# Performance work log

Measured on AMD Instinct MI355X. Metric: run time of the kernel, lower is better.

Reference implementation:

```python
import jax, jax.numpy as jnp
import numpy as np

B, T, S_ENC, D, H, E, K = 4, 1024, 64, 1024, 16, 8, 2
DK = D // H
HID = 4 * D
NEG = -65504.0
EPS = 1e-5


def rmsnorm(x, w):
    return w * (x * jax.lax.rsqrt(jnp.mean(x * x, axis=-1, keepdims=True) + EPS))


def mha(xq, xk, xv, mask, wq, wk, wv, wo):
    # linear (no bias): y = x @ W.T
    q = jnp.einsum('bsd,ed->bse', xq, wq).reshape(xq.shape[0], -1, H, DK).transpose(0, 2, 1, 3)
    k = jnp.einsum('bsd,ed->bse', xk, wk).reshape(xk.shape[0], -1, H, DK).transpose(0, 2, 1, 3)
    v = jnp.einsum('bsd,ed->bse', xv, wv).reshape(xv.shape[0], -1, H, DK).transpose(0, 2, 1, 3)
    scores = jnp.einsum('bhqd,bhkd->bhqk', q, k) / jnp.sqrt(jnp.float32(DK))
    scores = jnp.where(mask[:, None, :, :] == 0, NEG, scores)
    attn = jax.nn.softmax(scores, axis=-1)
    out = jnp.einsum('bhqk,bhkd->bhqd', attn, v)
    out = out.transpose(0, 2, 1, 3).reshape(xq.shape[0], -1, D)
    return jnp.einsum('bsd,ed->bse', out, wo)


def moe_ffn(x, gate_w, exp_w1, exp_w2, sh_w1, sh_w2):
    b, s, d = x.shape
    xf = x.reshape(-1, d)                                     # [N, D]
    # shared expert
    sh = jnp.einsum('nd,hd->nh', xf, sh_w1)
    sh = jax.nn.silu(sh)
    sh = jnp.einsum('nh,dh->nd', sh, sh_w2)
    # gating
    logits = jnp.einsum('nd,ed->ne', xf, gate_w)              # [N, E]
    topk_vals, topk_idx = jax.lax.top_k(logits, K)
    topk_gates = jax.nn.softmax(topk_vals, axis=-1)
    n = xf.shape[0]
    gates = jnp.zeros((n, E), dtype=xf.dtype).at[jnp.arange(n)[:, None], topk_idx].set(topk_gates)
    # all experts computed densely (as in the torch code), then gated
    h = jnp.einsum('nd,ehd->neh', xf, exp_w1)                 # [N, E, 4D]
    h = jax.nn.silu(h)
    eo = jnp.einsum('neh,edh->ned', h, exp_w2)                # [N, E, D]
    sel = jnp.einsum('ned,ne->nd', eo, gates)
    return (sh + sel).reshape(b, s, d)


def setup_inputs() -> dict:
    key = jax.random.key(0)
    ks = jax.random.split(key, 16)
    sd = 1.0 / np.sqrt(D)
    inp = {
        'x': jax.random.normal(ks[0], (B, T, D), jnp.float32),
        'encoder_output': jax.random.normal(ks[1], (B, S_ENC, D), jnp.float32),
        'tgt_mask': jnp.tril(jnp.ones((T, T), jnp.int32))[None].repeat(B, 0),
        'src_mask': jnp.ones((B, T, S_ENC), jnp.int32),
        'norm1_w': jnp.ones((D,), jnp.float32),
        'norm2_w': jnp.ones((D,), jnp.float32),
        'norm3_w': jnp.ones((D,), jnp.float32),
        'sa_wq': jax.random.normal(ks[2], (D, D), jnp.float32) * sd,
        'sa_wk': jax.random.normal(ks[3], (D, D), jnp.float32) * sd,
        'sa_wv': jax.random.normal(ks[4], (D, D), jnp.float32) * sd,
        'sa_wo': jax.random.normal(ks[5], (D, D), jnp.float32) * sd,
        'ca_wq': jax.random.normal(ks[6], (D, D), jnp.float32) * sd,
        'ca_wk': jax.random.normal(ks[7], (D, D), jnp.float32) * sd,
        'ca_wv': jax.random.normal(ks[8], (D, D), jnp.float32) * sd,
        'ca_wo': jax.random.normal(ks[9], (D, D), jnp.float32) * sd,
        'gate_w': jax.random.normal(ks[10], (E, D), jnp.float32) * 0.02,
        'exp_w1': jax.random.normal(ks[11], (E, HID, D), jnp.float32) * sd,
        'exp_w2': jax.random.normal(ks[12], (E, D, HID), jnp.float32) / np.sqrt(HID),
        'sh_w1': jax.random.normal(ks[13], (HID, D), jnp.float32) * sd,
        'sh_w2': jax.random.normal(ks[14], (D, HID), jnp.float32) / np.sqrt(HID),
    }
    return inp


def reference(x, encoder_output, tgt_mask, src_mask, norm1_w, norm2_w, norm3_w,
              sa_wq, sa_wk, sa_wv, sa_wo, ca_wq, ca_wk, ca_wv, ca_wo,
              gate_w, exp_w1, exp_w2, sh_w1, sh_w2):
    xn = rmsnorm(x, norm1_w)
    h = x + mha(xn, xn, xn, tgt_mask, sa_wq, sa_wk, sa_wv, sa_wo)
    hn = rmsnorm(h, norm2_w)
    h = h + mha(hn, encoder_output, encoder_output, src_mask, ca_wq, ca_wk, ca_wv, ca_wo)
    hn = rmsnorm(h, norm3_w)
    return h + moe_ffn(hn, gate_w, exp_w1, exp_w2, sh_w1, sh_w2)
```

## Files before the change

### kernel.cpp

```cpp
#include <hip/hip_runtime.h>
#include <hip/hip_bf16.h>
#include <cstdint>
#include <cstddef>
#include <math.h>

typedef __attribute__((ext_vector_type(8))) short bf16x8;
typedef __attribute__((ext_vector_type(4))) float f32x4;
typedef __attribute__((ext_vector_type(4))) short s16x4;

static __device__ __forceinline__ short f2bf(float f) {
  union { __hip_bfloat16 b; short s; } u;
  u.b = __float2bfloat16(f);
  return u.s;
}

static __device__ __forceinline__ float bf2f(short s) {
  union { unsigned u; float f; } v;
  v.u = ((unsigned)(unsigned short)s) << 16;
  return v.f;
}

static __device__ __forceinline__ void gload_lds16(const short* g, short* l) {
  __builtin_amdgcn_global_load_lds((const __attribute__((address_space(1))) void*)g,
                                   (__attribute__((address_space(3))) void*)l,
                                   16, 0, 0);
}

__global__ __launch_bounds__(256) void cvt_k(const float* __restrict__ src,
                                             short* __restrict__ dst, long n4) {
  long i = (long)blockIdx.x * blockDim.x + threadIdx.x;
  long stride = (long)gridDim.x * blockDim.x;
  for (; i < n4; i += stride) {
    float4 v = ((const float4*)src)[i];
    s16x4 o;
    o.x = f2bf(v.x); o.y = f2bf(v.y); o.z = f2bf(v.z); o.w = f2bf(v.w);
    ((s16x4*)dst)[i] = o;
  }
}

__global__ __launch_bounds__(256) void cvt2_k(const float* __restrict__ src,
                                              short* __restrict__ hi,
                                              short* __restrict__ lo, long n4) {
  long i = (long)blockIdx.x * blockDim.x + threadIdx.x;
  long stride = (long)gridDim.x * blockDim.x;
  for (; i < n4; i += stride) {
    float4 v = ((const float4*)src)[i];
    s16x4 h, l;
    h.x = f2bf(v.x); l.x = f2bf(v.x - bf2f(h.x));
    h.y = f2bf(v.y); l.y = f2bf(v.y - bf2f(h.y));
    h.z = f2bf(v.z); l.z = f2bf(v.z - bf2f(h.z));
    h.w = f2bf(v.w); l.w = f2bf(v.w - bf2f(h.w));
    ((s16x4*)hi)[i] = h;
    ((s16x4*)lo)[i] = l;
  }
}

__global__ __launch_bounds__(256) void rms2_k(const float* __restrict__ x,
                                              const float* __restrict__ w,
                                              short* __restrict__ hi,
                                              short* __restrict__ lo) {
  const int row = blockIdx.x, tid = threadIdx.x;
  const float* xr = x + (size_t)row * 1024;
  float4 v = *(const float4*)&xr[tid * 4];
  float ss = v.x * v.x + v.y * v.y + v.z * v.z + v.w * v.w;
#pragma unroll
  for (int off = 32; off; off >>= 1) ss += __shfl_down(ss, off);
  __shared__ float red[4];
  if ((tid & 63) == 0) red[tid >> 6] = ss;
  __syncthreads();
  float rs = rsqrtf((red[0] + red[1] + red[2] + red[3]) * (1.f / 1024.f) + 1e-5f);
  float4 wv = *(const float4*)&w[tid * 4];
  float o0 = v.x * rs * wv.x, o1 = v.y * rs * wv.y;
  float o2 = v.z * rs * wv.z, o3 = v.w * rs * wv.w;
  s16x4 h, l;
  h.x = f2bf(o0); l.x = f2bf(o0 - bf2f(h.x));
  h.y = f2bf(o1); l.y = f2bf(o1 - bf2f(h.y));
  h.z = f2bf(o2); l.z = f2bf(o2 - bf2f(h.z));
  h.w = f2bf(o3); l.w = f2bf(o3 - bf2f(h.w));
  const size_t ib = (size_t)row * 1024 + tid * 4;
  *(s16x4*)&hi[ib] = h;
  *(s16x4*)&lo[ib] = l;
}

__global__ __launch_bounds__(256) void rms_k(const float* __restrict__ x,
                                             const float* __restrict__ w,
                                             short* __restrict__ obf) {
  const int row = blockIdx.x, tid = threadIdx.x;
  const float* xr = x + (size_t)row * 1024;
  float4 v = *(const float4*)&xr[tid * 4];
  float ss = v.x * v.x + v.y * v.y + v.z * v.z + v.w * v.w;
#pragma unroll
  for (int off = 32; off; off >>= 1) ss += __shfl_down(ss, off);
  __shared__ float red[4];
  if ((tid & 63) == 0) red[tid >> 6] = ss;
  __syncthreads();
  float rs = rsqrtf((red[0] + red[1] + red[2] + red[3]) * (1.f / 1024.f) + 1e-5f);
  float4 wv = *(const float4*)&w[tid * 4];
  s16x4 ob;
  ob.x = f2bf(v.x * rs * wv.x); ob.y = f2bf(v.y * rs * wv.y);
  ob.z = f2bf(v.z * rs * wv.z); ob.w = f2bf(v.w * rs * wv.w);
  *(s16x4*)&obf[(size_t)row * 1024 + tid * 4] = ob;
}

template <int EPI>
__global__ __launch_bounds__(256)
void gemm3_k(const short* __restrict__ Ah, const short* __restrict__ Al,
             const short* __restrict__ Bh, const short* __restrict__ Bl,
             float* __restrict__ C, const float* __restrict__ resid,
             short* __restrict__ Ch, short* __restrict__ Cl,
             int M, int N, int K) {
  __shared__ short sAh[128 * 32];
  __shared__ short sAl[128 * 32];
  __shared__ short sBh[128 * 32];
  __shared__ short sBl[128 * 32];

  const int bn = blockIdx.x, bm = blockIdx.y;
  const int tid = threadIdx.x;
  const int lane = tid & 63, wv = tid >> 6;
  const int rch = lane >> 2;
  const int cch = (((lane & 3) ^ (rch & 3)) << 3);
  const int wr = wv >> 1, wc = wv & 1;
  const int lr = lane & 15, lg = lane >> 4;
  const int c0 = wv * 2, c1 = wv * 2 + 1;
  const int sw = ((lg ^ (lr & 3)) << 3);

  const int ra0 = bm * 128 + c0 * 16 + rch;
  const int ra1 = bm * 128 + c1 * 16 + rch;
  const int rb0 = bn * 128 + c0 * 16 + rch, rb1 = bn * 128 + c1 * 16 + rch;

  f32x4 acc[4][4];
#pragma unroll
  for (int m = 0; m < 4; m++)
#pragma unroll
    for (int n = 0; n < 4; n++) acc[m][n] = (f32x4){0.f, 0.f, 0.f, 0.f};

  const int nk = K >> 5;
  for (int kt = 0; kt < nk; ++kt) {
    __syncthreads();
    const int colk = (kt << 5) + cch;
    gload_lds16(Ah + (size_t)ra0 * K + colk, &sAh[c0 * 512]);
    gload_lds16(Ah + (size_t)ra1 * K + colk, &sAh[c1 * 512]);
    gload_lds16(Al + (size_t)ra0 * K + colk, &sAl[c0 * 512]);
    gload_lds16(Al + (size_t)ra1 * K + colk, &sAl[c1 * 512]);
    gload_lds16(Bh + (size_t)rb0 * K + colk, &sBh[c0 * 512]);
    gload_lds16(Bh + (size_t)rb1 * K + colk, &sBh[c1 * 512]);
    gload_lds16(Bl + (size_t)rb0 * K + colk, &sBl[c0 * 512]);
    gload_lds16(Bl + (size_t)rb1 * K + colk, &sBl[c1 * 512]);
    __syncthreads();
    bf16x8 ah[4], al[4], bh[4], bl[4];
#pragma unroll
    for (int m = 0; m < 4; m++) {
      const int o = (wr * 64 + m * 16 + lr) * 32 + sw;
      ah[m] = *(const bf16x8*)&sAh[o];
      al[m] = *(const bf16x8*)&sAl[o];
    }
#pragma unroll
    for (int n = 0; n < 4; n++) {
      const int o = (wc * 64 + n * 16 + lr) * 32 + sw;
      bh[n] = *(const bf16x8*)&sBh[o];
      bl[n] = *(const bf16x8*)&sBl[o];
    }
#pragma unroll
    for (int m = 0; m < 4; m++)
#pragma unroll
      for (int n = 0; n < 4; n++) {
        acc[m][n] = __builtin_amdgcn_mfma_f32_16x16x32_bf16(ah[m], bh[n], acc[m][n], 0, 0, 0);
        acc[m][n] = __builtin_amdgcn_mfma_f32_16x16x32_bf16(al[m], bh[n], acc[m][n], 0, 0, 0);
        acc[m][n] = __builtin_amdgcn_mfma_f32_16x16x32_bf16(ah[m], bl[n], acc[m][n], 0, 0, 0);
      }
  }

  const int cbase = bn * 128 + wc * 64;
#pragma unroll
  for (int m = 0; m < 4; m++) {
    const int rl = bm * 128 + wr * 64 + m * 16 + lg * 4;
#pragma unroll
    for (int n = 0; n < 4; n++) {
      f32x4 v = acc[m][n];
      const int col = cbase + n * 16 + lr;
#pragma unroll
      for (int j = 0; j < 4; j++) {
        const size_t idx = (size_t)(rl + j) * N + col;
        if (EPI == 0) {
          C[idx] = v[j];
        } else if (EPI == 2) {
          C[idx] = v[j] + resid[idx];
        } else {
          short hh = f2bf(v[j]);
          Ch[idx] = hh;
          Cl[idx] = f2bf(v[j] - bf2f(hh));
        }
      }
    }
  }
}

template <bool CAUSAL>
__global__ __launch_bounds__(256)
void attn3_k(const short* __restrict__ Qh, const short* __restrict__ Ql, int ldq,
             const short* __restrict__ Kh, const short* __restrict__ Kl, int ldk,
             const short* __restrict__ Vh, const short* __restrict__ Vl, int ldv,
             short* __restrict__ Oh, short* __restrict__ Ol, int ldo,
             int Tq, int Tkv, float scale) {
  __shared__ short sQh[64 * 72], sQl[64 * 72];
  __shared__ short sKh[64 * 72], sKl[64 * 72];
  __shared__ short sVh[64 * 72], sVl[64 * 72];
  __shared__ short sPh[4][16 * 72], sPl[4][16 * 72];

  const int idx = blockIdx.x;
  const int qb = 15 - (idx >> 6);
  const int h = (idx >> 2) & 15;
  const int b = idx & 3;
  const int tid = threadIdx.x, lane = tid & 63, wv = tid >> 6;
  const int hoff = h * 64;
  const int lr = lane & 15, lg = lane >> 4;
  const int qlo = wv * 16;

#pragma unroll
  for (int j = 0; j < 2; j++) {
    int c = j * 256 + tid;
    int row = c >> 3, col = (c & 7) << 3;
    size_t g = (size_t)(b * Tq + qb * 64 + row) * ldq + hoff + col;
    *(bf16x8*)&sQh[row * 72 + col] = *(const bf16x8*)&Qh[g];
    *(bf16x8*)&sQl[row * 72 + col] = *(const bf16x8*)&Ql[g];
  }

  float m_run = -1e30f, l_run = 0.f;
  f32x4 o[4];
#pragma unroll
  for (int n = 0; n < 4; n++) o[n] = (f32x4){0.f, 0.f, 0.f, 0.f};

  const int ntiles = CAUSAL ? (qb + 1) : (Tkv >> 6);
  for (int kt = 0; kt < ntiles; ++kt) {
    __syncthreads();
#pragma unroll
    for (int j = 0; j < 2; j++) {
      int c = j * 256 + tid;
      int row = c >> 3, col = (c & 7) << 3;
      size_t gk = (size_t)(b * Tkv + kt * 64 + row) * ldk + hoff + col;
      *(bf16x8*)&sKh[row * 72 + col] = *(const bf16x8*)&Kh[gk];
      *(bf16x8*)&sKl[row * 72 + col] = *(const bf16x8*)&Kl[gk];
      size_t gv = (size_t)(b * Tkv + kt * 64 + row) * ldv + hoff + col;
      bf16x8 vh = *(const bf16x8*)&Vh[gv];
      bf16x8 vl = *(const bf16x8*)&Vl[gv];
#pragma unroll
      for (int i = 0; i < 8; i++) {
        sVh[(col + i) * 72 + row] = vh[i];
        sVl[(col + i) * 72 + row] = vl[i];
      }
    }
    __syncthreads();

    f32x4 st[4];
#pragma unroll
    for (int jk = 0; jk < 4; jk++) st[jk] = (f32x4){0.f, 0.f, 0.f, 0.f};
#pragma unroll
    for (int ks = 0; ks < 2; ks++) {
      bf16x8 qh = *(const bf16x8*)&sQh[(qlo + lr) * 72 + ks * 32 + lg * 8];
      bf16x8 ql = *(const bf16x8*)&sQl[(qlo + lr) * 72 + ks * 32 + lg * 8];
#pragma unroll
      for (int jk = 0; jk < 4; jk++) {
        const int o2 = (jk * 16 + lr) * 72 + ks * 32 + lg * 8;
        bf16x8 kh = *(const bf16x8*)&sKh[o2];
        bf16x8 kl = *(const bf16x8*)&sKl[o2];
        st[jk] = __builtin_amdgcn_mfma_f32_16x16x32_bf16(kh, qh, st[jk], 0, 0, 0);
        st[jk] = __builtin_amdgcn_mfma_f32_16x16x32_bf16(kl, qh, st[jk], 0, 0, 0);
        st[jk] = __builtin_amdgcn_mfma_f32_16x16x32_bf16(kh, ql, st[jk], 0, 0, 0);
      }
    }

    const int qg = qb * 64 + qlo + lr;
    float s[16];
    float tmax = -1e30f;
#pragma unroll
    for (int jk = 0; jk < 4; jk++)
#pragma unroll
      for (int r2 = 0; r2 < 4; r2++) {
        float xv = st[jk][r2] * scale;
        if (CAUSAL && kt == qb) {
          int kvidx = kt * 64 + jk * 16 + lg * 4 + r2;
          if (kvidx > qg) xv = -1e30f;
        }
        s[jk * 4 + r2] = xv;
        tmax = fmaxf(tmax, xv);
      }
    tmax = fmaxf(tmax, __shfl_xor(tmax, 16));
    tmax = fmaxf(tmax, __shfl_xor(tmax, 32));
    float m_new = fmaxf(m_run, tmax);
    float alpha = __expf(m_run - m_new);
    float tsum = 0.f;
#pragma unroll
    for (int i = 0; i < 16; i++) {
      float ev = (s[i] <= -1e29f) ? 0.f : __expf(s[i] - m_new);
      s[i] = ev;
      tsum += ev;
    }
    tsum += __shfl_xor(tsum, 16);
    tsum += __shfl_xor(tsum, 32);
    l_run = l_run * alpha + tsum;
    m_run = m_new;

    short* pwh = &sPh[wv][0];
    short* pwl = &sPl[wv][0];
#pragma unroll
    for (int jk = 0; jk < 4; jk++) {
      s16x4 ph, pl;
      float e0 = s[jk * 4 + 0], e1 = s[jk * 4 + 1], e2 = s[jk * 4 + 2], e3 = s[jk * 4 + 3];
      ph.x = f2bf(e0); pl.x = f2bf(e0 - bf2f(ph.x));
      ph.y = f2bf(e1); pl.y = f2bf(e1 - bf2f(ph.y));
      ph.z = f2bf(e2); pl.z = f2bf(e2 - bf2f(ph.z));
      ph.w = f2bf(e3); pl.w = f2bf(e3 - bf2f(ph.w));
      *(s16x4*)&pwh[lr * 72 + jk * 16 + lg * 4] = ph;
      *(s16x4*)&pwl[lr * 72 + jk * 16 + lg * 4] = pl;
    }
#pragma unroll
    for (int r2 = 0; r2 < 4; r2++) {
      float al = __shfl(alpha, lg * 4 + r2);
#pragma unroll
      for (int db = 0; db < 4; db++) o[db][r2] *= al;
    }
    __syncthreads();

#pragma unroll
    for (int ks = 0; ks < 2; ks++) {
      bf16x8 pah = *(const bf16x8*)&pwh[lr * 72 + ks * 32 + lg * 8];
      bf16x8 pal = *(const bf16x8*)&pwl[lr * 72 + ks * 32 + lg * 8];
#pragma unroll
      for (int db = 0; db < 4; db++) {
        const int o2 = (db * 16 + lr) * 72 + ks * 32 + lg * 8;
        bf16x8 vfh = *(const bf16x8*)&sVh[o2];
        bf16x8 vfl = *(const bf16x8*)&sVl[o2];
        o[db] = __builtin_amdgcn_mfma_f32_16x16x32_bf16(pah, vfh, o[db], 0, 0, 0);
        o[db] = __builtin_amdgcn_mfma_f32_16x16x32_bf16(pal, vfh, o[db], 0, 0, 0);
        o[db] = __builtin_amdgcn_mfma_f32_16x16x32_bf16(pah, vfl, o[db], 0, 0, 0);
      }
    }
  }

  float rinv = 1.f / l_run;
#pragma unroll
  for (int r2 = 0; r2 < 4; r2++) {
    float inv = __shfl(rinv, lg * 4 + r2);
    int token = b * Tq + qb * 64 + qlo + lg * 4 + r2;
#pragma unroll
    for (int db = 0; db < 4; db++) {
      float vv = o[db][r2] * inv;
      short hh = f2bf(vv);
      const size_t ob = (size_t)token * ldo + hoff + db * 16 + lr;
      Oh[ob] = hh;
      Ol[ob] = f2bf(vv - bf2f(hh));
    }
  }
}

template <int EPI, int MODE>
__global__ __launch_bounds__(256)
void gemm_bt_k(const short* __restrict__ A, const short* __restrict__ B,
               void* C, int M, int N, int K,
               const int* __restrict__ row_map,
               const int* __restrict__ counts,
               const int* __restrict__ offs) {
  __shared__ short sA[128 * 64];
  __shared__ short sB[128 * 64];
  __shared__ int sRow[128];

  const int tid = threadIdx.x;
  const int bn = blockIdx.x, bm = blockIdx.y;
  const int e = blockIdx.z;
  const int cnt = counts[e];
  const int base = offs[e];
  if (bm * 128 >= cnt) return;
  const short* Bp = B + (size_t)e * N * K;

  const int lane = tid & 63, wv = tid >> 6;
  const int lrow = lane >> 3;
  const int lcc = ((lane & 7) ^ lrow) << 3;
  const int wr = wv >> 1, wc = wv & 1;
  const int lr = lane & 15, lg = lane >> 4;

  if (MODE == 1) {
    if (tid < 128) {
      int r = bm * 128 + tid;
      sRow[tid] = (r < cnt) ? row_map[base + r] : row_map[base];
    }
    __syncthreads();
  }
  int rag[4], rbg[4];
#pragma unroll
  for (int i = 0; i < 4; i++) {
    const int rl = wv * 32 + i * 8 + lrow;
    if (MODE == 2) {
      rag[i] = base + ((bm * 128 + rl < cnt) ? (bm * 128 + rl) : 0);
    } else {
      rag[i] = sRow[rl];
    }
    rbg[i] = bn * 128 + rl;
  }

  f32x4 acc[4][4];
#pragma unroll
  for (int m = 0; m < 4; m++)
#pragma unroll
    for (int n = 0; n < 4; n++) acc[m][n] = (f32x4){0.f, 0.f, 0.f, 0.f};

  const int nk = K >> 6;
  for (int kt = 0; kt < nk; ++kt) {
    __syncthreads();
    const int colk = (kt << 6) + lcc;
#pragma unroll
    for (int i = 0; i < 4; i++) {
      gload_lds16(A + (size_t)rag[i] * K + colk, &sA[(wv * 32 + i * 8) * 64]);
      gload_lds16(Bp + (size_t)rbg[i] * K + colk, &sB[(wv * 32 + i * 8) * 64]);
    }
    __syncthreads();
#pragma unroll
    for (int ks = 0; ks < 2; ks++) {
      bf16x8 a[4], b[4];
#pragma unroll
      for (int m = 0; m < 4; m++) {
        const int rr = wr * 64 + m * 16 + lr;
        a[m] = *(const bf16x8*)&sA[rr * 64 + ((((ks << 2) + lg) ^ (lr & 7)) << 3)];
      }
#pragma unroll
      for (int n = 0; n < 4; n++) {
        const int rr = wc * 64 + n * 16 + lr;
        b[n] = *(const bf16x8*)&sB[rr * 64 + ((((ks << 2) + lg) ^ (lr & 7)) << 3)];
      }
#pragma unroll
      for (int m = 0; m < 4; m++)
#pragma unroll
        for (int n = 0; n < 4; n++)
          acc[m][n] = __builtin_amdgcn_mfma_f32_16x16x32_bf16(a[m], b[n], acc[m][n], 0, 0, 0);
    }
  }

  const int cbase = bn * 128 + wc * 64;
#pragma unroll
  for (int m = 0; m < 4; m++) {
    const int rl = wr * 64 + m * 16 + lg * 4;
#pragma unroll
    for (int n = 0; n < 4; n++) {
      f32x4 v = acc[m][n];
      const int col = cbase + n * 16 + lr;
#pragma unroll
      for (int j = 0; j < 4; j++) {
        const int rloc = bm * 128 + rl + j;
        if (rloc >= cnt) continue;
        const size_t idx = (size_t)(base + rloc) * N + col;
        float xv = v[j];
        if (EPI == 1) {
          float s = xv / (1.f + __expf(-xv));
          ((short*)C)[idx] = f2bf(s);
        } else {
          ((short*)C)[idx] = f2bf(xv);
        }
      }
    }
  }
}

__global__ __launch_bounds__(256) void gate_k(const float* __restrict__ H,
                                              const float* __restrict__ w3,
                                              const float* __restrict__ gw,
                                              int* counts, int* tok_e, int* tok_s,
                                              float* tok_g) {
  const int token = blockIdx.x * 4 + (threadIdx.x >> 6);
  const int lane = threadIdx.x & 63;
  const float* xr = H + (size_t)token * 1024;
  double a[8] = {0, 0, 0, 0, 0, 0, 0, 0};
  double ss = 0.0;
#pragma unroll
  for (int i = 0; i < 4; i++) {
    float4 xv = *(const float4*)&xr[i * 256 + lane * 4];
    float4 w3v = *(const float4*)&w3[i * 256 + lane * 4];
    ss += (double)xv.x * xv.x + (double)xv.y * xv.y + (double)xv.z * xv.z + (double)xv.w * xv.w;
    double xw0 = (double)xv.x * (double)w3v.x, xw1 = (double)xv.y * (double)w3v.y;
    double xw2 = (double)xv.z * (double)w3v.z, xw3 = (double)xv.w * (double)w3v.w;
#pragma unroll
    for (int e = 0; e < 8; e++) {
      float4 wv = *(const float4*)&gw[e * 1024 + i * 256 + lane * 4];
      a[e] += xw0 * wv.x + xw1 * wv.y + xw2 * wv.z + xw3 * wv.w;
    }
  }
#pragma unroll
  for (int off = 32; off; off >>= 1) {
    ss += __shfl_down(ss, off);
#pragma unroll
    for (int e = 0; e < 8; e++) a[e] += __shfl_down(a[e], off);
  }
  if (lane == 0) {
    double v0 = a[0]; int i0 = 0;
#pragma unroll
    for (int e = 1; e < 8; e++) if (a[e] > v0) { v0 = a[e]; i0 = e; }
    double v1 = -1e300; int i1 = 0;
#pragma unroll
    for (int e = 0; e < 8; e++) if (e != i0 && a[e] > v1) { v1 = a[e]; i1 = e; }
    double rs = 1.0 / sqrt(ss * (1.0 / 1024.0) + 1e-5);
    double t = exp((v1 - v0) * rs);
    double g0 = 1.0 / (1.0 + t);
    int s0 = atomicAdd(&counts[i0], 1);
    int s1 = atomicAdd(&counts[i1], 1);
    tok_e[2 * token] = i0; tok_e[2 * token + 1] = i1;
    tok_s[2 * token] = s0; tok_s[2 * token + 1] = s1;
    tok_g[2 * token] = (float)g0; tok_g[2 * token + 1] = (float)(1.0 - g0);
  }
}

__global__ void offsets_k(int* counts, int* offs) {
  if (threadIdx.x == 0 && blockIdx.x == 0) {
    counts[8] = 4096;
    int s = 0;
    for (int e = 0; e < 9; e++) { offs[e] = s; s += counts[e]; }
  }
}

__global__ __launch_bounds__(256) void build_rows_k(const int* __restrict__ offs,
                                                    const int* __restrict__ tok_e,
                                                    const int* __restrict__ tok_s,
                                                    int* __restrict__ row_map,
                                                    int* __restrict__ tok_row) {
  int n = blockIdx.x * 256 + threadIdx.x;
  int e0 = tok_e[2 * n], e1 = tok_e[2 * n + 1];
  int r0 = offs[e0] + tok_s[2 * n], r1 = offs[e1] + tok_s[2 * n + 1];
  row_map[r0] = n; row_map[r1] = n;
  row_map[8192 + n] = n;
  tok_row[2 * n] = r0; tok_row[2 * n + 1] = r1;
}

__global__ __launch_bounds__(256) void combine_k(const float* __restrict__ H,
                                                 const short* __restrict__ eo,
                                                 const int* __restrict__ tok_row,
                                                 const float* __restrict__ tok_g,
                                                 float* __restrict__ out) {
  const int n = blockIdx.x, t = threadIdx.x;
  const int r0 = tok_row[2 * n], r1 = tok_row[2 * n + 1];
  const float g0 = tok_g[2 * n], g1 = tok_g[2 * n + 1];
  const size_t ib = (size_t)n * 1024 + t * 4;
  float4 hv = *(const float4*)&H[ib];
  s16x4 sv = *(const s16x4*)&eo[(size_t)(8192 + n) * 1024 + t * 4];
  s16x4 a0 = *(const s16x4*)&eo[(size_t)r0 * 1024 + t * 4];
  s16x4 a1 = *(const s16x4*)&eo[(size_t)r1 * 1024 + t * 4];
  float4 ov;
  ov.x = hv.x + bf2f(sv.x) + g0 * bf2f(a0.x) + g1 * bf2f(a1.x);
  ov.y = hv.y + bf2f(sv.y) + g0 * bf2f(a0.y) + g1 * bf2f(a1.y);
  ov.z = hv.z + bf2f(sv.z) + g0 * bf2f(a0.z) + g1 * bf2f(a1.z);
  ov.w = hv.w + bf2f(sv.w) + g0 * bf2f(a0.w) + g1 * bf2f(a1.w);
  *(float4*)&out[ib] = ov;
}

extern "C" void kernel_launch(void* const* d_in, const int* in_sizes, int n_in,
                              void* d_out, int out_size, void* d_ws, size_t ws_size,
                              hipStream_t stream) {
  (void)in_sizes; (void)n_in; (void)out_size;
  const float* x     = (const float*)d_in[0];
  const float* enc   = (const float*)d_in[1];
  const float* n1w   = (const float*)d_in[4];
  const float* n2w   = (const float*)d_in[5];
  const float* n3w   = (const float*)d_in[6];
  const float* sa_wq = (const float*)d_in[7];
  const float* sa_wk = (const float*)d_in[8];
  const float* sa_wv = (const float*)d_in[9];
  const float* sa_wo = (const float*)d_in[10];
  const float* ca_wq = (const float*)d_in[11];
  const float* ca_wk = (const float*)d_in[12];
  const float* ca_wv = (const float*)d_in[13];
  const float* ca_wo = (const float*)d_in[14];
  const float* gw    = (const float*)d_in[15];
  const float* e_w1  = (const float*)d_in[16];
  const float* e_w2  = (const float*)d_in[17];
  const float* s_w1  = (const float*)d_in[18];
  const float* s_w2  = (const float*)d_in[19];
  float* out = (float*)d_out;

  char* p = (char*)d_ws;
  size_t off = 0;
  auto alloc = [&](size_t bytes) -> void* {
    void* r = p + off;
    off += (bytes + 255) & ~(size_t)255;
    return r;
  };
  short* w_all1 = (short*)alloc(9LL * 4096 * 1024 * 2);
  short* w_all2 = (short*)alloc(9LL * 1024 * 4096 * 2);
  short* xn     = (short*)alloc(4096LL * 1024 * 2);
  char*  U      = (char*)alloc(12288LL * 4096 * 2);
  short* hbuf   = (short*)U;
  float* Hb     = (float*)alloc(4096LL * 1024 * 4);
  short* eo     = (short*)alloc(12288LL * 1024 * 2);
  short* xh     = (short*)alloc(4096LL * 1024 * 2);
  short* xl     = (short*)alloc(4096LL * 1024 * 2);
  short* ench   = (short*)alloc(256LL * 1024 * 2);
  short* encl   = (short*)alloc(256LL * 1024 * 2);
  short* wsh    = (short*)alloc(3072LL * 1024 * 2);
  short* wsl    = (short*)alloc(3072LL * 1024 * 2);
  int*   counts = (int*)alloc(9 * 4);
  int*   offs   = (int*)alloc(9 * 4);
  int*   tok_e  = (int*)alloc(4096LL * 2 * 4);
  int*   tok_s  = (int*)alloc(4096LL * 2 * 4);
  float* tok_g  = (float*)alloc(4096LL * 2 * 4);
  int*   tok_row= (int*)alloc(4096LL * 2 * 4);
  int*   row_map= (int*)alloc(12288LL * 4);
  if (off > ws_size) return;

  short* qkvh = (short*)U;
  short* qkvl = qkvh + 4096LL * 3072;
  short* crossQh = (short*)U;
  short* crossQl = crossQh + 4096LL * 1024;
  short* encKVh  = crossQl + 4096LL * 1024;
  short* encKVl  = encKVh + 256LL * 2048;

  auto cvt = [&](const float* s, short* d, long n) {
    long n4 = n / 4;
    long g = (n4 + 255) / 256;
    int grid = (int)(g > 4096 ? 4096 : g);
    cvt_k<<<grid, 256, 0, stream>>>(s, d, n4);
  };
  auto cvt2 = [&](const float* s, short* h, short* l, long n) {
    long n4 = n / 4;
    long g = (n4 + 255) / 256;
    int grid = (int)(g > 4096 ? 4096 : g);
    cvt2_k<<<grid, 256, 0, stream>>>(s, h, l, n4);
  };

  cvt(e_w1, w_all1, 8L * 4096 * 1024);
  cvt(s_w1, w_all1 + 8L * 4096 * 1024, 4096L * 1024);
  cvt(e_w2, w_all2, 8L * 1024 * 4096);
  cvt(s_w2, w_all2 + 8L * 1024 * 4096, 1024L * 4096);
  cvt2(enc, ench, encl, 256L * 1024);

  rms2_k<<<4096, 256, 0, stream>>>(x, n1w, xh, xl);
  cvt2(sa_wq, wsh, wsl, 1024L * 1024);
  cvt2(sa_wk, wsh + 1048576, wsl + 1048576, 1024L * 1024);
  cvt2(sa_wv, wsh + 2097152, wsl + 2097152, 1024L * 1024);
  gemm3_k<3><<<dim3(24, 32), 256, 0, stream>>>(xh, xl, wsh, wsl, nullptr, nullptr,
      qkvh, qkvl, 4096, 3072, 1024);
  attn3_k<true><<<1024, 256, 0, stream>>>(qkvh, qkvl, 3072,
      qkvh + 1024, qkvl + 1024, 3072, qkvh + 2048, qkvl + 2048, 3072,
      xh, xl, 1024, 1024, 1024, 0.125f);
  cvt2(sa_wo, wsh, wsl, 1024L * 1024);
  gemm3_k<2><<<dim3(8, 32), 256, 0, stream>>>(xh, xl, wsh, wsl, Hb, x,
      nullptr, nullptr, 4096, 1024, 1024);

  rms2_k<<<4096, 256, 0, stream>>>(Hb, n2w, xh, xl);
  cvt2(ca_wq, wsh, wsl, 1024L * 1024);
  gemm3_k<3><<<dim3(8, 32), 256, 0, stream>>>(xh, xl, wsh, wsl, nullptr, nullptr,
      crossQh, crossQl, 4096, 1024, 1024);
  cvt2(ca_wk, wsh, wsl, 1024L * 1024);
  cvt2(ca_wv, wsh + 1048576, wsl + 1048576, 1024L * 1024);
  gemm3_k<3><<<dim3(16, 2), 256, 0, stream>>>(ench, encl, wsh, wsl, nullptr, nullptr,
      encKVh, encKVl, 256, 2048, 1024);
  attn3_k<false><<<1024, 256, 0, stream>>>(crossQh, crossQl, 1024,
      encKVh, encKVl, 2048, encKVh + 1024, encKVl + 1024, 2048,
      xh, xl, 1024, 1024, 64, 0.125f);
  cvt2(ca_wo, wsh, wsl, 1024L * 1024);
  gemm3_k<2><<<dim3(8, 32), 256, 0, stream>>>(xh, xl, wsh, wsl, Hb, Hb,
      nullptr, nullptr, 4096, 1024, 1024);

  rms_k<<<4096, 256, 0, stream>>>(Hb, n3w, xn);
  hipMemsetAsync(counts, 0, 8 * sizeof(int), stream);
  gate_k<<<1024, 256, 0, stream>>>(Hb, n3w, gw, counts, tok_e, tok_s, tok_g);
  offsets_k<<<1, 1, 0, stream>>>(counts, offs);
  build_rows_k<<<16, 256, 0, stream>>>(offs, tok_e, tok_s, row_map, tok_row);
  gemm_bt_k<1, 1><<<dim3(32, 32, 9), 256, 0, stream>>>(xn, w_all1, hbuf,
      4096, 4096, 1024, row_map, counts, offs);
  gemm_bt_k<3, 2><<<dim3(8, 32, 9), 256, 0, stream>>>(hbuf, w_all2, eo,
      4096, 1024, 4096, row_map, counts, offs);

  combine_k<<<4096, 256, 0, stream>>>(Hb, eo, tok_row, tok_g, out);
}
```

Measured before the change: 977.6 us.

## Use 512-thread MoE GEMM blocks and keep attention Q fragments in registers

The MoE expert GEMM kernel moves from 4 to 8 waves per 128x128 tile. Each wave now computes a 64x32 sub-tile with half the accumulators, and the loads to shared memory are spread across more threads. Separately, the attention kernel loads its Q fragments straight from global memory into registers and drops the shared-memory Q staging buffers. This cuts LDS use per block and the per-wave register pressure. In exchange, the GEMM reads more A fragments from shared memory per MFMA, and 512-thread blocks may limit how blocks are scheduled per CU.

```diff
diff --git a/kernel.cpp b/kernel.cpp
--- a/kernel.cpp
+++ b/kernel.cpp
@@ -202,7 +202,6 @@
              const short* __restrict__ Vh, const short* __restrict__ Vl, int ldv,
              short* __restrict__ Oh, short* __restrict__ Ol, int ldo,
              int Tq, int Tkv, float scale) {
-  __shared__ short sQh[64 * 72], sQl[64 * 72];
   __shared__ short sKh[64 * 72], sKl[64 * 72];
   __shared__ short sVh[64 * 72], sVl[64 * 72];
   __shared__ short sPh[4][16 * 72], sPl[4][16 * 72];
@@ -216,13 +215,14 @@
   const int lr = lane & 15, lg = lane >> 4;
   const int qlo = wv * 16;
 
-#pragma unroll
-  for (int j = 0; j < 2; j++) {
-    int c = j * 256 + tid;
-    int row = c >> 3, col = (c & 7) << 3;
-    size_t g = (size_t)(b * Tq + qb * 64 + row) * ldq + hoff + col;
-    *(bf16x8*)&sQh[row * 72 + col] = *(const bf16x8*)&Qh[g];
-    *(bf16x8*)&sQl[row * 72 + col] = *(const bf16x8*)&Ql[g];
+  bf16x8 qhf[2], qlf[2];
+  {
+    const size_t qrow = (size_t)(b * Tq + qb * 64 + qlo + lr) * ldq + hoff;
+#pragma unroll
+    for (int ks = 0; ks < 2; ks++) {
+      qhf[ks] = *(const bf16x8*)&Qh[qrow + ks * 32 + lg * 8];
+      qlf[ks] = *(const bf16x8*)&Ql[qrow + ks * 32 + lg * 8];
+    }
   }
 
   float m_run = -1e30f, l_run = 0.f;
@@ -256,16 +256,14 @@
     for (int jk = 0; jk < 4; jk++) st[jk] = (f32x4){0.f, 0.f, 0.f, 0.f};
 #pragma unroll
     for (int ks = 0; ks < 2; ks++) {
-      bf16x8 qh = *(const bf16x8*)&sQh[(qlo + lr) * 72 + ks * 32 + lg * 8];
-      bf16x8 ql = *(const bf16x8*)&sQl[(qlo + lr) * 72 + ks * 32 + lg * 8];
 #pragma unroll
       for (int jk = 0; jk < 4; jk++) {
         const int o2 = (jk * 16 + lr) * 72 + ks * 32 + lg * 8;
         bf16x8 kh = *(const bf16x8*)&sKh[o2];
         bf16x8 kl = *(const bf16x8*)&sKl[o2];
-        st[jk] = __builtin_amdgcn_mfma_f32_16x16x32_bf16(kh, qh, st[jk], 0, 0, 0);
-        st[jk] = __builtin_amdgcn_mfma_f32_16x16x32_bf16(kl, qh, st[jk], 0, 0, 0);
-        st[jk] = __builtin_amdgcn_mfma_f32_16x16x32_bf16(kh, ql, st[jk], 0, 0, 0);
+        st[jk] = __builtin_amdgcn_mfma_f32_16x16x32_bf16(kh, qhf[ks], st[jk], 0, 0, 0);
+        st[jk] = __builtin_amdgcn_mfma_f32_16x16x32_bf16(kl, qhf[ks], st[jk], 0, 0, 0);
+        st[jk] = __builtin_amdgcn_mfma_f32_16x16x32_bf16(kh, qlf[ks], st[jk], 0, 0, 0);
       }
     }
 
@@ -354,7 +352,7 @@
 }
 
 template <int EPI, int MODE>
-__global__ __launch_bounds__(256)
+__global__ __launch_bounds__(512)
 void gemm_bt_k(const short* __restrict__ A, const short* __restrict__ B,
                void* C, int M, int N, int K,
                const int* __restrict__ row_map,
@@ -372,11 +370,11 @@
   if (bm * 128 >= cnt) return;
   const short* Bp = B + (size_t)e * N * K;
 
-  const int lane = tid & 63, wv = tid >> 6;
+  const int lane = tid & 63, wid = tid >> 6;
+  const int wr = wid >> 2, wc = wid & 3;
+  const int lr = lane & 15, lg = lane >> 4;
   const int lrow = lane >> 3;
   const int lcc = ((lane & 7) ^ lrow) << 3;
-  const int wr = wv >> 1, wc = wv & 1;
-  const int lr = lane & 15, lg = lane >> 4;
 
   if (MODE == 1) {
     if (tid < 128) {
@@ -385,10 +383,10 @@
     }
     __syncthreads();
   }
-  int rag[4], rbg[4];
-#pragma unroll
-  for (int i = 0; i < 4; i++) {
-    const int rl = wv * 32 + i * 8 + lrow;
+  int rag[2], rbg[2];
+#pragma unroll
+  for (int i = 0; i < 2; i++) {
+    const int rl = wid * 8 + i * 64 + lrow;
     if (MODE == 2) {
       rag[i] = base + ((bm * 128 + rl < cnt) ? (bm * 128 + rl) : 0);
     } else {
@@ -397,51 +395,47 @@
     rbg[i] = bn * 128 + rl;
   }
 
-  f32x4 acc[4][4];
+  f32x4 acc[4][2];
 #pragma unroll
   for (int m = 0; m < 4; m++)
 #pragma unroll
-    for (int n = 0; n < 4; n++) acc[m][n] = (f32x4){0.f, 0.f, 0.f, 0.f};
+    for (int n = 0; n < 2; n++) acc[m][n] = (f32x4){0.f, 0.f, 0.f, 0.f};
 
   const int nk = K >> 6;
   for (int kt = 0; kt < nk; ++kt) {
     __syncthreads();
     const int colk = (kt << 6) + lcc;
 #pragma unroll
-    for (int i = 0; i < 4; i++) {
-      gload_lds16(A + (size_t)rag[i] * K + colk, &sA[(wv * 32 + i * 8) * 64]);
-      gload_lds16(Bp + (size_t)rbg[i] * K + colk, &sB[(wv * 32 + i * 8) * 64]);
+    for (int i = 0; i < 2; i++) {
+      gload_lds16(A + (size_t)rag[i] * K + colk, &sA[(wid * 8 + i * 64) * 64]);
+      gload_lds16(Bp + (size_t)rbg[i] * K + colk, &sB[(wid * 8 + i * 64) * 64]);
     }
     __syncthreads();
 #pragma unroll
     for (int ks = 0; ks < 2; ks++) {
-      bf16x8 a[4], b[4];
-#pragma unroll
-      for (int m = 0; m < 4; m++) {
-        const int rr = wr * 64 + m * 16 + lr;
-        a[m] = *(const bf16x8*)&sA[rr * 64 + ((((ks << 2) + lg) ^ (lr & 7)) << 3)];
-      }
-#pragma unroll
-      for (int n = 0; n < 4; n++) {
-        const int rr = wc * 64 + n * 16 + lr;
-        b[n] = *(const bf16x8*)&sB[rr * 64 + ((((ks << 2) + lg) ^ (lr & 7)) << 3)];
-      }
+      const int sw = ((((ks << 2) + lg) ^ (lr & 7)) << 3);
+      bf16x8 a[4], b[2];
 #pragma unroll
       for (int m = 0; m < 4; m++)
-#pragma unroll
-        for (int n = 0; n < 4; n++)
+        a[m] = *(const bf16x8*)&sA[(wr * 64 + m * 16 + lr) * 64 + sw];
+#pragma unroll
+      for (int n = 0; n < 2; n++)
+        b[n] = *(const bf16x8*)&sB[(wc * 32 + n * 16 + lr) * 64 + sw];
+#pragma unroll
+      for (int m = 0; m < 4; m++)
+#pragma unroll
+        for (int n = 0; n < 2; n++)
           acc[m][n] = __builtin_amdgcn_mfma_f32_16x16x32_bf16(a[m], b[n], acc[m][n], 0, 0, 0);
     }
   }
 
-  const int cbase = bn * 128 + wc * 64;
 #pragma unroll
   for (int m = 0; m < 4; m++) {
     const int rl = wr * 64 + m * 16 + lg * 4;
 #pragma unroll
-    for (int n = 0; n < 4; n++) {
+    for (int n = 0; n < 2; n++) {
       f32x4 v = acc[m][n];
-      const int col = cbase + n * 16 + lr;
+      const int col = bn * 128 + wc * 32 + n * 16 + lr;
 #pragma unroll
       for (int j = 0; j < 4; j++) {
         const int rloc = bm * 128 + rl + j;
@@ -660,9 +654,9 @@
   gate_k<<<1024, 256, 0, stream>>>(Hb, n3w, gw, counts, tok_e, tok_s, tok_g);
   offsets_k<<<1, 1, 0, stream>>>(counts, offs);
   build_rows_k<<<16, 256, 0, stream>>>(offs, tok_e, tok_s, row_map, tok_row);
-  gemm_bt_k<1, 1><<<dim3(32, 32, 9), 256, 0, stream>>>(xn, w_all1, hbuf,
+  gemm_bt_k<1, 1><<<dim3(32, 32, 9), 512, 0, stream>>>(xn, w_all1, hbuf,
       4096, 4096, 1024, row_map, counts, offs);
-  gemm_bt_k<3, 2><<<dim3(8, 32, 9), 256, 0, stream>>>(hbuf, w_all2, eo,
+  gemm_bt_k<3, 2><<<dim3(8, 32, 9), 512, 0, stream>>>(hbuf, w_all2, eo,
       4096, 1024, 4096, row_map, counts, offs);
 
   combine_k<<<4096, 256, 0, stream>>>(Hb, eo, tok_row, tok_g, out);
```

Measured after the change: 951.1 us. 2.7% less time.
